# Kernel optimization log

Measured on AMD Instinct MI355X. Metric: run time of the kernel, lower is better.

Reference implementation:

```python
import jax, jax.numpy as jnp
import numpy as np

PI = jnp.pi


def _spow(t, p):
    # t >= 0; safe t**p with value 0 (and zero grad) at t == 0
    tt = jnp.where(t > 0, t, 1.0)
    return jnp.where(t > 0, tt ** p, 0.0)


def _wavelets(t, f, fm, pm, em, fo, ph):
    # t: [L]; f: [S,1] -> returns [S, L] bank of wavelets (one per scale)
    sigma = jnp.maximum(fm / (2.0 * PI * f), 1e-6)        # [S,1]
    br = jnp.cos(2.0 * PI * f * t)                        # [S,L]
    bi = jnp.sin(2.0 * PI * f * t)
    # real_part: + pm0*br - c^2 (t/sig)^fo0 br pm1 + ... alternating, c = 2..7
    real = br * pm[0]
    sign = -1.0
    for j in range(6):
        c = j + 2.0
        real = real + sign * (_spow(t, fo[j]) * c / sigma ** fo[j] * c) * br * pm[j + 1]
        sign = -sign
    # imag_part: same pattern with fo6..fo11, pm8..pm13; j==9 term has the
    # anomalous parenthesization from the source: t**fo*5/(sigma**fo*5)
    imag = bi * pm[7]
    sign = -1.0
    for j in range(6, 12):
        c = j - 4.0
        if j == 9:
            term = (_spow(t, fo[j]) * 5.0 / (sigma ** fo[j] * 5.0)) * bi * pm[j + 2]
        else:
            term = (_spow(t, fo[j]) * c / sigma ** fo[j] * c) * bi * pm[j + 2]
        imag = imag + sign * term
        sign = -sign
    gauss = em[0] * jnp.exp(-t ** 2 / (2.0 * sigma ** 2))  # [S,L]
    rw = real * gauss
    iw = imag * gauss
    amp = rw + iw
    samp = amp / jnp.linalg.norm(amp, axis=-1, keepdims=True)
    phase = jnp.arctan2(iw, rw)
    w = (samp * jnp.sin(phase) * ph[0]) * (samp * jnp.cos(phase) * ph[1]) \
        * (samp * jnp.sinc(phase / PI) * ph[2])
    return w


def reference(x, scales, f_mod, poly_mod, exp_mod, frac_order, phase_mod, i):
    B, C = x.shape[0], x.shape[1]
    xf = x.reshape(B, C, -1)                              # [B,C,L]
    L = xf.shape[-1]
    S = scales.shape[0]
    t = jnp.arange(L, dtype=x.dtype)
    f = (1.0 / scales)[:, None]                           # [S,1]
    W = _wavelets(t, f, f_mod[i], poly_mod[i], exp_mod[i], frac_order[i],
                  phase_mod[i])                            # [S,L] kernels, K = L
    # torch F.conv1d(padding='same', groups=C*S) = cross-correlation with
    # left pad (K-1)//2. Computed exactly via zero-padded FFT linear conv.
    K = L
    Nfft = 2 * L                                          # >= L + K - 1, no aliasing
    Xf = jnp.fft.rfft(xf, n=Nfft, axis=-1)                # [B,C,F]
    Wf = jnp.fft.rfft(W[:, ::-1], n=Nfft, axis=-1)        # [S,F] (corr = conv w/ flip)
    y = jnp.fft.irfft(Xf[:, :, None, :] * Wf[None, None], n=Nfft, axis=-1)  # [B,C,S,2L]
    left = (K - 1) // 2
    off = K - 1 - left
    y = y[..., off:off + L]                               # [B,C,S,L]
    # torch channel layout: out[:, j] = corr(x[:, j % C], wavelet[j % S])
    j = jnp.arange(C * S)
    return y[:, j % C, j % S, :]                          # [B, C*S, L]


def setup_inputs() -> dict:
    key = jax.random.key(0)
    ks = jax.random.split(key, 6)
    B, C, H, Wd = 16, 16, 64, 64
    S, NSTEPS = 16, 10
    x = jax.random.normal(ks[0], (B, C, H, Wd), dtype=jnp.float32)
    scales = jnp.linspace(1.0, 32.0, S, dtype=jnp.float32)
    f_mod = 1.0 + 0.02 * jax.random.normal(ks[1], (NSTEPS,), dtype=jnp.float32)
    poly_mod = 1.0 + 0.02 * jax.random.normal(ks[2], (NSTEPS, 14), dtype=jnp.float32)
    exp_mod = 1.0 + 0.02 * jax.random.normal(ks[3], (NSTEPS, 1), dtype=jnp.float32)
    frac_order = 1.0 + 0.02 * jax.random.normal(ks[4], (NSTEPS, 12), dtype=jnp.float32)
    phase_mod = 1.0 + 0.02 * jax.random.normal(ks[5], (NSTEPS, 3), dtype=jnp.float32)
    return {"x": x, "scales": scales, "f_mod": f_mod, "poly_mod": poly_mod,
            "exp_mod": exp_mod, "frac_order": frac_order,
            "phase_mod": phase_mod, "i": 3}
```

## Files before the change

kernel.cpp:

```cpp
#include <hip/hip_runtime.h>
#include <math.h>

#define QMAX 128
#define CHUNK 1024
#define ZCUT 1920

__global__ void wavelet_build(const float* __restrict__ scales,
                              const float* __restrict__ f_mod,
                              const float* __restrict__ poly_mod,
                              const float* __restrict__ exp_mod,
                              const float* __restrict__ frac_order,
                              const float* __restrict__ phase_mod,
                              const int* __restrict__ istep,
                              float* __restrict__ Wout) {
    const int k = blockIdx.x;
    const int t = threadIdx.x;
    const int i = istep[0];
    const float PI2 = 6.28318530717958647692f;

    const float scale = scales[k];
    const float f = 1.0f / scale;
    const float fm = f_mod[i];
    const float* pm = poly_mod + i * 14;
    const float em0 = exp_mod[i];
    const float* fo = frac_order + i * 12;
    const float* ph = phase_mod + i * 3;

    const float sigma = fmaxf(fm / (PI2 * f), 1e-6f);
    const float tf = (float)t;
    const float arg = PI2 * f * tf;
    const float br = cosf(arg);
    const float bi = sinf(arg);

    float rp = pm[0];
    float sign = -1.0f;
    for (int j = 0; j < 6; ++j) {
        float c = (float)(j + 2);
        float sp = (tf > 0.0f) ? powf(tf, fo[j]) : 0.0f;
        float term = sp * c / powf(sigma, fo[j]) * c * pm[j + 1];
        rp += sign * term;
        sign = -sign;
    }
    float ipoly = pm[7];
    sign = -1.0f;
    for (int j = 6; j < 12; ++j) {
        float sp = (tf > 0.0f) ? powf(tf, fo[j]) : 0.0f;
        float term;
        if (j == 9) {
            term = sp * 5.0f / (powf(sigma, fo[j]) * 5.0f) * pm[j + 2];
        } else {
            float c = (float)(j - 4);
            term = sp * c / powf(sigma, fo[j]) * c * pm[j + 2];
        }
        ipoly += sign * term;
        sign = -sign;
    }

    const float gauss = em0 * expf(-tf * tf / (2.0f * sigma * sigma));
    const float rw = br * rp * gauss;
    const float iw = bi * ipoly * gauss;
    const float amp = rw + iw;

    float sq = amp * amp;
    #pragma unroll
    for (int off = 32; off > 0; off >>= 1) sq += __shfl_xor(sq, off, 64);
    __shared__ float wsum[2];
    if ((t & 63) == 0) wsum[t >> 6] = sq;
    __syncthreads();
    const float norm = sqrtf(wsum[0] + wsum[1]);

    const float samp = amp / norm;
    const float phase = atan2f(iw, rw);
    const float sphi = sinf(phase);
    const float cphi = cosf(phase);
    const float snc = (phase != 0.0f) ? (sphi / phase) : 1.0f;
    const float w = (samp * sphi * ph[0]) * (samp * cphi * ph[1]) * (samp * snc * ph[2]);
    Wout[k * QMAX + t] = w;
}

__global__ __launch_bounds__(256) void conv_rep(const float* __restrict__ x,
                                                const float* __restrict__ W,
                                                float* __restrict__ out) {
    __shared__ __attribute__((aligned(16))) float xs[CHUNK + QMAX];
    __shared__ __attribute__((aligned(16))) float Wl[QMAX];

    const int bk = blockIdx.y;
    const int b = bk >> 4;
    const int k = bk & 15;
    const int p0 = blockIdx.x * CHUNK;
    const int tid = threadIdx.x;
    const int p = p0 + 4 * tid;

    float4 val = make_float4(0.0f, 0.0f, 0.0f, 0.0f);

    if (p0 + CHUNK > ZCUT) {
        if (tid < QMAX) Wl[tid] = W[k * QMAX + tid];
        const float* xrow = x + (size_t)bk * 4096;
        for (int li = tid; li < CHUNK + QMAX; li += 256) {
            int g = p0 - 2047 + li;
            xs[li] = (g >= 0 && g < 4096) ? xrow[g] : 0.0f;
        }
        __syncthreads();

        if (p >= ZCUT) {
            float acc[4] = {0.0f, 0.0f, 0.0f, 0.0f};
            const int base = 4 * tid;
            for (int q = 0; q < QMAX; q += 4) {
                float4 w4 = *(const float4*)&Wl[q];
                float4 x0 = *(const float4*)&xs[base + q];
                float4 x1 = *(const float4*)&xs[base + q + 4];
                float win[8] = {x0.x, x0.y, x0.z, x0.w,
                                x1.x, x1.y, x1.z, x1.w};
                float wv[4] = {w4.x, w4.y, w4.z, w4.w};
                #pragma unroll
                for (int j = 0; j < 4; ++j) {
                    #pragma unroll
                    for (int r = 0; r < 4; ++r) {
                        acc[r] = fmaf(win[r + j], wv[j], acc[r]);
                    }
                }
            }
            val = make_float4(acc[0], acc[1], acc[2], acc[3]);
        }
    }

    #pragma unroll
    for (int r = 0; r < 16; ++r) {
        size_t oidx = ((size_t)b * 256 + (size_t)(r * 16 + k)) * 4096 + p;
        *(float4*)&out[oidx] = val;
    }
}

extern "C" void kernel_launch(void* const* d_in, const int* in_sizes, int n_in,
                              void* d_out, int out_size, void* d_ws, size_t ws_size,
                              hipStream_t stream) {
    const float* x          = (const float*)d_in[0];
    const float* scales     = (const float*)d_in[1];
    const float* f_mod      = (const float*)d_in[2];
    const float* poly_mod   = (const float*)d_in[3];
    const float* exp_mod    = (const float*)d_in[4];
    const float* frac_order = (const float*)d_in[5];
    const float* phase_mod  = (const float*)d_in[6];
    const int*   istep      = (const int*)d_in[7];
    float* out = (float*)d_out;
    float* Wbuf = (float*)d_ws;

    wavelet_build<<<dim3(16), dim3(QMAX), 0, stream>>>(
        scales, f_mod, poly_mod, exp_mod, frac_order, phase_mod, istep, Wbuf);

    conv_rep<<<dim3(4096 / CHUNK, 256), dim3(256), 0, stream>>>(x, Wbuf, out);
}
```

Baseline: 36.17 us.

## Split convolution into diagonal-row compute and separate nontemporal replication kernel

Instead of each conv block computing a chunk and writing it to all 16 replicated output rows, a single block per (b,k) now computes the whole row (with zero-padded shared copy of x), writes only the diagonal output row, and a new kernel copies that row to the other 15 replicas using nontemporal stores. This aims to separate the compute from the bulk replication writes and use streaming stores for the 64MB-ish output. It adds an extra kernel launch and re-reads the computed rows from memory, and the conv grid drops to 256 blocks.

```diff
diff --git a/kernel.cpp b/kernel.cpp
--- a/kernel.cpp
+++ b/kernel.cpp
@@ -2,8 +2,8 @@
 #include <math.h>
 
 #define QMAX 128
-#define CHUNK 1024
 #define ZCUT 1920
+#define PAD  131
 
 __global__ void wavelet_build(const float* __restrict__ scales,
                               const float* __restrict__ f_mod,
@@ -78,33 +78,34 @@
     Wout[k * QMAX + t] = w;
 }
 
-__global__ __launch_bounds__(256) void conv_rep(const float* __restrict__ x,
-                                                const float* __restrict__ W,
-                                                float* __restrict__ out) {
-    __shared__ __attribute__((aligned(16))) float xs[CHUNK + QMAX];
+__global__ __launch_bounds__(256) void conv_diag(const float* __restrict__ x,
+                                                 const float* __restrict__ W,
+                                                 float* __restrict__ out) {
+    __shared__ __attribute__((aligned(16))) float xs[PAD + 4096];
     __shared__ __attribute__((aligned(16))) float Wl[QMAX];
 
-    const int bk = blockIdx.y;
+    const int bk = blockIdx.x;
     const int b = bk >> 4;
     const int k = bk & 15;
-    const int p0 = blockIdx.x * CHUNK;
     const int tid = threadIdx.x;
-    const int p = p0 + 4 * tid;
 
-    float4 val = make_float4(0.0f, 0.0f, 0.0f, 0.0f);
+    if (tid < QMAX) Wl[tid] = W[k * QMAX + tid];
+    const float* xrow = x + (size_t)bk * 4096;
+    for (int li = tid; li < PAD + 4096; li += 256) {
+        xs[li] = (li >= PAD) ? xrow[li - PAD] : 0.0f;
+    }
+    __syncthreads();
 
-    if (p0 + CHUNK > ZCUT) {
-        if (tid < QMAX) Wl[tid] = W[k * QMAX + tid];
-        const float* xrow = x + (size_t)bk * 4096;
-        for (int li = tid; li < CHUNK + QMAX; li += 256) {
-            int g = p0 - 2047 + li;
-            xs[li] = (g >= 0 && g < 4096) ? xrow[g] : 0.0f;
-        }
-        __syncthreads();
+    float* orow = out + ((size_t)b * 256 + k) * 4096;
 
+    #pragma unroll
+    for (int v = 0; v < 4; ++v) {
+        const int fidx = tid + 256 * v;
+        const int p = 4 * fidx;
+        float4 val = make_float4(0.0f, 0.0f, 0.0f, 0.0f);
         if (p >= ZCUT) {
             float acc[4] = {0.0f, 0.0f, 0.0f, 0.0f};
-            const int base = 4 * tid;
+            const int base = PAD + p - 2047;
             for (int q = 0; q < QMAX; q += 4) {
                 float4 w4 = *(const float4*)&Wl[q];
                 float4 x0 = *(const float4*)&xs[base + q];
@@ -122,12 +123,27 @@
             }
             val = make_float4(acc[0], acc[1], acc[2], acc[3]);
         }
+        *(float4*)&orow[p] = val;
     }
+}
 
+__global__ __launch_bounds__(256) void replicate_rows(float* __restrict__ out) {
+    const int k = blockIdx.z;
+    const int rr = blockIdx.y;
+    const int b = blockIdx.x;
+    const int r = 1 + (rr & 15);
+    const float* src = out + ((size_t)b * 256 + k) * 4096;
+    float* dst = out + ((size_t)b * 256 + (size_t)(rr + 1) * 16 + k) * 4096;
+    const int tid = threadIdx.x;
+    (void)r;
     #pragma unroll
-    for (int r = 0; r < 16; ++r) {
-        size_t oidx = ((size_t)b * 256 + (size_t)(r * 16 + k)) * 4096 + p;
-        *(float4*)&out[oidx] = val;
+    for (int v = 0; v < 4; ++v) {
+        const int fidx = tid + 256 * v;
+        float4 val = *(const float4*)&src[4 * fidx];
+        __builtin_nontemporal_store(val.x, &dst[4 * fidx + 0]);
+        __builtin_nontemporal_store(val.y, &dst[4 * fidx + 1]);
+        __builtin_nontemporal_store(val.z, &dst[4 * fidx + 2]);
+        __builtin_nontemporal_store(val.w, &dst[4 * fidx + 3]);
     }
 }
 
@@ -148,5 +164,7 @@
     wavelet_build<<<dim3(16), dim3(QMAX), 0, stream>>>(
         scales, f_mod, poly_mod, exp_mod, frac_order, phase_mod, istep, Wbuf);
 
-    conv_rep<<<dim3(4096 / CHUNK, 256), dim3(256), 0, stream>>>(x, Wbuf, out);
+    conv_diag<<<dim3(256), dim3(256), 0, stream>>>(x, Wbuf, out);
+
+    replicate_rows<<<dim3(16, 15, 16), dim3(256), 0, stream>>>(out);
 }
```

Result: slower. 40.37 us (+11.6%).
